# Performance work log

Hardware: AMD Instinct MI355X
Metric: run time of the kernel (lower is better)

Reference implementation:

```python
import jax, jax.numpy as jnp
import numpy as np

N_NODES = 50000
N_EDGES = 800000
HID = 128
LAYERS = 3


def setup_inputs() -> dict:
    key = jax.random.key(0)
    k1, k2, k3, k4 = jax.random.split(key, 4)
    x = jax.random.normal(k1, (N_NODES, HID), dtype=jnp.float32)
    edge_index = jax.random.randint(k2, (2, N_EDGES), 0, N_NODES, dtype=jnp.int64)
    # Glorot-ish scale so 3 stacked layers stay numerically tame
    Ws = jax.random.normal(k3, (LAYERS, HID, HID), dtype=jnp.float32) * (1.0 / np.sqrt(HID))
    bs = jax.random.normal(k4, (LAYERS, HID), dtype=jnp.float32) * 0.01
    return {"x": x, "edge_index": edge_index, "Ws": Ws, "bs": bs}


def reference(x, edge_index, Ws, bs):
    """Stacked GCNConv (add_self_loops=False): out = D^-1/2 A D^-1/2 (x W) + b.
    Returns (final_x, embeddings_list) like the torch module."""
    N = x.shape[0]
    src = edge_index[0]  # message sources (x_j)
    dst = edge_index[1]  # aggregation targets
    # gcn_norm with unit edge weights, no self loops: in-degree on targets
    deg = jax.ops.segment_sum(jnp.ones(src.shape[0], dtype=x.dtype), dst, num_segments=N)
    dinv = jnp.where(deg > 0, jax.lax.rsqrt(jnp.maximum(deg, 1.0)), 0.0).astype(x.dtype)
    norm = dinv[src] * dinv[dst]  # [E]

    embeddings = [x]
    for l in range(Ws.shape[0]):
        h = x @ Ws[l]                               # [N, D] dense transform
        msg = h[src] * norm[:, None]                # [E, D] gather + normalize
        x = jax.ops.segment_sum(msg, dst, num_segments=N) + bs[l]  # scatter-add
        embeddings.append(x)
    return (x, embeddings)
```

## Files before the change

kernel.cpp:

```cpp
#include <hip/hip_runtime.h>

#define N_NODES 50000
#define N_EDGES 800000
#define HID 128
#define SLOT (N_NODES * HID)
#define W_STRIDE (HID * HID)

#define OFF_CNT    0ul
#define OFF_DINV   200192ul
#define OFF_RPTR   400384ul
#define OFF_RFILL  600576ul
#define OFF_BSUM   800768ul
#define OFF_BOFS   801280ul
#define OFF_SRCS   801792ul


__global__ void k_zero_cnt(int* __restrict__ cnt) {
    int i = blockIdx.x * blockDim.x + threadIdx.x;
    if (i < N_NODES) cnt[i] = 0;
}

__global__ void k_count(const int* __restrict__ ei, int* __restrict__ cnt) {
    int e = blockIdx.x * blockDim.x + threadIdx.x;
    if (e < N_EDGES) {
        int d = ei[N_EDGES + e];
        atomicAdd(&cnt[d], 1);
    }
}

__global__ void k_dinv(const int* __restrict__ cnt, float* __restrict__ dinv) {
    int i = blockIdx.x * blockDim.x + threadIdx.x;
    if (i < N_NODES) {
        int c = cnt[i];
        dinv[i] = (c > 0) ? rsqrtf((float)c) : 0.0f;
    }
}

__global__ void k_scan_block(const int* __restrict__ cnt, int* __restrict__ rptr,
                             int* __restrict__ bsum) {
    __shared__ int s[512];
    int tid = threadIdx.x;
    int gid = blockIdx.x * 512 + tid;
    int v = (gid < N_NODES) ? cnt[gid] : 0;
    s[tid] = v;
    __syncthreads();
    for (int off = 1; off < 512; off <<= 1) {
        int t = (tid >= off) ? s[tid - off] : 0;
        __syncthreads();
        s[tid] += t;
        __syncthreads();
    }
    if (gid < N_NODES) rptr[gid] = s[tid] - v;
    if (tid == 511) bsum[blockIdx.x] = s[511];
}

__global__ void k_scan_sums(const int* __restrict__ bsum, int* __restrict__ bofs, int nb) {
    __shared__ int s[128];
    int tid = threadIdx.x;
    int v = (tid < nb) ? bsum[tid] : 0;
    s[tid] = v;
    __syncthreads();
    for (int off = 1; off < 128; off <<= 1) {
        int t = (tid >= off) ? s[tid - off] : 0;
        __syncthreads();
        s[tid] += t;
        __syncthreads();
    }
    if (tid < nb) bofs[tid] = s[tid] - v;
}

__global__ void k_scan_add(int* __restrict__ rptr, int* __restrict__ rfill,
                           const int* __restrict__ bofs) {
    int gid = blockIdx.x * blockDim.x + threadIdx.x;
    if (gid < N_NODES) {
        int r = rptr[gid] + bofs[gid >> 9];
        rptr[gid] = r;
        rfill[gid] = r;
    }
    if (gid == 0) rptr[N_NODES] = N_EDGES;
}

__global__ void k_scatter(const int* __restrict__ ei, int* __restrict__ rfill,
                          int* __restrict__ srcs) {
    int e = blockIdx.x * blockDim.x + threadIdx.x;
    if (e < N_EDGES) {
        int sv = ei[e];
        int d  = ei[N_EDGES + e];
        int pos = atomicAdd(&rfill[d], 1);
        srcs[pos] = sv;
    }
}

__launch_bounds__(256, 2)
__global__ void k_gemm_scale(const float* __restrict__ X, const float* __restrict__ W,
                             const float* __restrict__ dinv, float* __restrict__ H) {
    __shared__ float sX[128 * HID];
    int tid = threadIdx.x;
    int row0 = blockIdx.x * 128;

    const float4* X4  = (const float4*)X;
    float4*       sX4 = (float4*)sX;
    for (int j = tid; j < 4096; j += 256) {
        int r   = j >> 5;
        int c4  = j & 31;
        int row = row0 + r;
        float4 v = {0.f, 0.f, 0.f, 0.f};
        if (row < N_NODES) v = X4[row * 32 + c4];
        sX4[r * 32 + (c4 ^ ((r >> 3) & 7))] = v;
    }
    __syncthreads();

    int ty  = tid >> 4;
    int tx  = tid & 15;
    int swz = ty & 7;

    float4 acc[8][2];
    #pragma unroll
    for (int r = 0; r < 8; ++r) {
        acc[r][0] = {0.f, 0.f, 0.f, 0.f};
        acc[r][1] = {0.f, 0.f, 0.f, 0.f};
    }

    const float4* W4 = (const float4*)W;

    #pragma unroll 2
    for (int k0 = 0; k0 < HID; k0 += 4) {
        int k4 = k0 >> 2;
        float4 xv[8];
        #pragma unroll
        for (int r = 0; r < 8; ++r)
            xv[r] = sX4[(ty * 8 + r) * 32 + (k4 ^ swz)];
        float4 wv[4][2];
        #pragma unroll
        for (int kk = 0; kk < 4; ++kk) {
            wv[kk][0] = W4[(k0 + kk) * 32 + tx * 2 + 0];
            wv[kk][1] = W4[(k0 + kk) * 32 + tx * 2 + 1];
        }
        #pragma unroll
        for (int r = 0; r < 8; ++r) {
            float xk0 = xv[r].x, xk1 = xv[r].y, xk2 = xv[r].z, xk3 = xv[r].w;
            #pragma unroll
            for (int hh = 0; hh < 2; ++hh) {
                acc[r][hh].x += xk0 * wv[0][hh].x + xk1 * wv[1][hh].x + xk2 * wv[2][hh].x + xk3 * wv[3][hh].x;
                acc[r][hh].y += xk0 * wv[0][hh].y + xk1 * wv[1][hh].y + xk2 * wv[2][hh].y + xk3 * wv[3][hh].y;
                acc[r][hh].z += xk0 * wv[0][hh].z + xk1 * wv[1][hh].z + xk2 * wv[2][hh].z + xk3 * wv[3][hh].z;
                acc[r][hh].w += xk0 * wv[0][hh].w + xk1 * wv[1][hh].w + xk2 * wv[2][hh].w + xk3 * wv[3][hh].w;
            }
        }
    }

    float4* H4 = (float4*)H;
    #pragma unroll
    for (int r = 0; r < 8; ++r) {
        int row = row0 + ty * 8 + r;
        if (row < N_NODES) {
            float dv = dinv[row];
            float4 o0 = acc[r][0], o1 = acc[r][1];
            o0.x *= dv; o0.y *= dv; o0.z *= dv; o0.w *= dv;
            o1.x *= dv; o1.y *= dv; o1.z *= dv; o1.w *= dv;
            H4[row * 32 + tx * 2 + 0] = o0;
            H4[row * 32 + tx * 2 + 1] = o1;
        }
    }
}

__global__ void k_agg(const float* __restrict__ H, const int* __restrict__ rptr,
                      const int* __restrict__ srcs, const float* __restrict__ dinv,
                      const float* __restrict__ bias, float* __restrict__ out0) {
    int wid  = (blockIdx.x * blockDim.x + threadIdx.x) >> 6;
    int lane = threadIdx.x & 63;
    if (wid >= N_NODES) return;

    int beg = rptr[wid];
    int end = rptr[wid + 1];

    float2 a0 = {0.f, 0.f}, a1 = {0.f, 0.f}, a2 = {0.f, 0.f}, a3 = {0.f, 0.f};
    int p  = beg;
    int n4 = beg + ((end - beg) & ~3);
    for (; p < n4; p += 4) {
        int s0 = srcs[p + 0];
        int s1 = srcs[p + 1];
        int s2 = srcs[p + 2];
        int s3 = srcs[p + 3];
        float2 h0 = *(const float2*)&H[s0 * HID + lane * 2];
        float2 h1 = *(const float2*)&H[s1 * HID + lane * 2];
        float2 h2 = *(const float2*)&H[s2 * HID + lane * 2];
        float2 h3 = *(const float2*)&H[s3 * HID + lane * 2];
        a0.x += h0.x; a0.y += h0.y;
        a1.x += h1.x; a1.y += h1.y;
        a2.x += h2.x; a2.y += h2.y;
        a3.x += h3.x; a3.y += h3.y;
    }
    for (; p < end; ++p) {
        int s = srcs[p];
        float2 hv = *(const float2*)&H[s * HID + lane * 2];
        a0.x += hv.x; a0.y += hv.y;
    }
    float dv  = dinv[wid];
    float2 bb = *(const float2*)&bias[lane * 2];
    float2 res;
    res.x = (a0.x + a1.x + a2.x + a3.x) * dv + bb.x;
    res.y = (a0.y + a1.y + a2.y + a3.y) * dv + bb.y;
    *(float2*)&out0[wid * HID + lane * 2] = res;
}

__global__ void k_copy(const float* __restrict__ src, float* __restrict__ dst, int n4) {
    int i = blockIdx.x * blockDim.x + threadIdx.x;
    if (i < n4) ((float4*)dst)[i] = ((const float4*)src)[i];
}


extern "C" void kernel_launch(void* const* d_in, const int* in_sizes, int n_in,
                              void* d_out, int out_size, void* d_ws, size_t ws_size,
                              hipStream_t stream) {
    const float* x  = (const float*)d_in[0];
    const int*   ei = (const int*)d_in[1];
    const float* Ws = (const float*)d_in[2];
    const float* bs = (const float*)d_in[3];
    float* out = (float*)d_out;
    char*  ws  = (char*)d_ws;

    int*   cnt   = (int*)  (ws + OFF_CNT);
    float* dinv  = (float*)(ws + OFF_DINV);
    int*   rptr  = (int*)  (ws + OFF_RPTR);
    int*   rfill = (int*)  (ws + OFF_RFILL);
    int*   bsum  = (int*)  (ws + OFF_BSUM);
    int*   bofs  = (int*)  (ws + OFF_BOFS);
    int*   srcs  = (int*)  (ws + OFF_SRCS);

    float* slot0 = out;
    float* slot1 = out + 1l * SLOT;
    float* slot2 = out + 2l * SLOT;
    float* slot3 = out + 3l * SLOT;
    float* slot4 = out + 4l * SLOT;
    float* h     = slot0;

    const int NB_NODE = (N_NODES + 255) / 256;
    const int NB_EDGE = (N_EDGES + 255) / 256;
    const int NB_SCAN = (N_NODES + 511) / 512;

    k_zero_cnt  <<<NB_NODE, 256, 0, stream>>>(cnt);
    k_count     <<<NB_EDGE, 256, 0, stream>>>(ei, cnt);
    k_dinv      <<<NB_NODE, 256, 0, stream>>>(cnt, dinv);
    k_scan_block<<<NB_SCAN, 512, 0, stream>>>(cnt, rptr, bsum);
    k_scan_sums <<<1, 128, 0, stream>>>(bsum, bofs, NB_SCAN);
    k_scan_add  <<<NB_NODE, 256, 0, stream>>>(rptr, rfill, bofs);
    k_scatter   <<<NB_EDGE, 256, 0, stream>>>(ei, rfill, srcs);

    k_copy<<<SLOT / 4 / 256, 256, 0, stream>>>(x, slot1, SLOT / 4);

    const int NB_GEMM = (N_NODES + 127) / 128;
    const int NB_AGG  = (N_NODES + 3) / 4;

    k_gemm_scale<<<NB_GEMM, 256, 0, stream>>>(x, Ws + 0 * W_STRIDE, dinv, h);
    k_agg       <<<NB_AGG, 256, 0, stream>>>(h, rptr, srcs, dinv, bs + 0 * HID, slot2);

    k_gemm_scale<<<NB_GEMM, 256, 0, stream>>>(slot2, Ws + 1 * W_STRIDE, dinv, h);
    k_agg       <<<NB_AGG, 256, 0, stream>>>(h, rptr, srcs, dinv, bs + 1 * HID, slot3);

    k_gemm_scale<<<NB_GEMM, 256, 0, stream>>>(slot3, Ws + 2 * W_STRIDE, dinv, h);
    k_agg       <<<NB_AGG, 256, 0, stream>>>(h, rptr, srcs, dinv, bs + 2 * HID, slot4);
    k_copy<<<SLOT / 4 / 256, 256, 0, stream>>>(slot4, slot0, SLOT / 4);
}
```

Baseline: 428.7 us.

## Use float4 half-wave aggregation, smaller GEMM tiles, and fuse final copy into aggregation

The aggregation kernel now splits each wavefront into two halves that gather float4 rows from different edges, then combines them with a cross-half shuffle. This is meant to raise memory-level parallelism and vector width on the gather. The GEMM tile drops to 64 rows per block with launch bounds of 4 to increase occupancy. When the workspace is large enough, H is placed there, and the last aggregation writes both output slots, which removes the final copy kernel. The cost is extra workspace use and an added fallback branch.

```diff
diff --git a/kernel.cpp b/kernel.cpp
--- a/kernel.cpp
+++ b/kernel.cpp
@@ -13,6 +13,7 @@
 #define OFF_BSUM   800768ul
 #define OFF_BOFS   801280ul
 #define OFF_SRCS   801792ul
+#define OFF_H_WS   4001792ul
 
 
 __global__ void k_zero_cnt(int* __restrict__ cnt) {
@@ -91,16 +92,16 @@
     }
 }
 
-__launch_bounds__(256, 2)
+__launch_bounds__(256, 4)
 __global__ void k_gemm_scale(const float* __restrict__ X, const float* __restrict__ W,
                              const float* __restrict__ dinv, float* __restrict__ H) {
-    __shared__ float sX[128 * HID];
+    __shared__ float sX[64 * HID];
     int tid = threadIdx.x;
-    int row0 = blockIdx.x * 128;
+    int row0 = blockIdx.x * 64;
 
     const float4* X4  = (const float4*)X;
     float4*       sX4 = (float4*)sX;
-    for (int j = tid; j < 4096; j += 256) {
+    for (int j = tid; j < 2048; j += 256) {
         int r   = j >> 5;
         int c4  = j & 31;
         int row = row0 + r;
@@ -112,11 +113,11 @@
 
     int ty  = tid >> 4;
     int tx  = tid & 15;
-    int swz = ty & 7;
-
-    float4 acc[8][2];
+    int swz = (ty >> 1) & 7;
+
+    float4 acc[4][2];
     #pragma unroll
-    for (int r = 0; r < 8; ++r) {
+    for (int r = 0; r < 4; ++r) {
         acc[r][0] = {0.f, 0.f, 0.f, 0.f};
         acc[r][1] = {0.f, 0.f, 0.f, 0.f};
     }
@@ -126,18 +127,18 @@
     #pragma unroll 2
     for (int k0 = 0; k0 < HID; k0 += 4) {
         int k4 = k0 >> 2;
-        float4 xv[8];
-        #pragma unroll
-        for (int r = 0; r < 8; ++r)
-            xv[r] = sX4[(ty * 8 + r) * 32 + (k4 ^ swz)];
         float4 wv[4][2];
         #pragma unroll
         for (int kk = 0; kk < 4; ++kk) {
             wv[kk][0] = W4[(k0 + kk) * 32 + tx * 2 + 0];
             wv[kk][1] = W4[(k0 + kk) * 32 + tx * 2 + 1];
         }
+        float4 xv[4];
         #pragma unroll
-        for (int r = 0; r < 8; ++r) {
+        for (int r = 0; r < 4; ++r)
+            xv[r] = sX4[(ty * 4 + r) * 32 + (k4 ^ swz)];
+        #pragma unroll
+        for (int r = 0; r < 4; ++r) {
             float xk0 = xv[r].x, xk1 = xv[r].y, xk2 = xv[r].z, xk3 = xv[r].w;
             #pragma unroll
             for (int hh = 0; hh < 2; ++hh) {
@@ -151,8 +152,8 @@
 
     float4* H4 = (float4*)H;
     #pragma unroll
-    for (int r = 0; r < 8; ++r) {
-        int row = row0 + ty * 8 + r;
+    for (int r = 0; r < 4; ++r) {
+        int row = row0 + ty * 4 + r;
         if (row < N_NODES) {
             float dv = dinv[row];
             float4 o0 = acc[r][0], o1 = acc[r][1];
@@ -166,42 +167,75 @@
 
 __global__ void k_agg(const float* __restrict__ H, const int* __restrict__ rptr,
                       const int* __restrict__ srcs, const float* __restrict__ dinv,
-                      const float* __restrict__ bias, float* __restrict__ out0) {
+                      const float* __restrict__ bias, float* __restrict__ out0,
+                      float* __restrict__ out1) {
     int wid  = (blockIdx.x * blockDim.x + threadIdx.x) >> 6;
     int lane = threadIdx.x & 63;
     if (wid >= N_NODES) return;
+    int half = lane >> 5;
+    int l32  = lane & 31;
 
     int beg = rptr[wid];
     int end = rptr[wid + 1];
-
-    float2 a0 = {0.f, 0.f}, a1 = {0.f, 0.f}, a2 = {0.f, 0.f}, a3 = {0.f, 0.f};
-    int p  = beg;
-    int n4 = beg + ((end - beg) & ~3);
-    for (; p < n4; p += 4) {
-        int s0 = srcs[p + 0];
-        int s1 = srcs[p + 1];
-        int s2 = srcs[p + 2];
-        int s3 = srcs[p + 3];
-        float2 h0 = *(const float2*)&H[s0 * HID + lane * 2];
-        float2 h1 = *(const float2*)&H[s1 * HID + lane * 2];
-        float2 h2 = *(const float2*)&H[s2 * HID + lane * 2];
-        float2 h3 = *(const float2*)&H[s3 * HID + lane * 2];
-        a0.x += h0.x; a0.y += h0.y;
-        a1.x += h1.x; a1.y += h1.y;
-        a2.x += h2.x; a2.y += h2.y;
-        a3.x += h3.x; a3.y += h3.y;
-    }
-    for (; p < end; ++p) {
-        int s = srcs[p];
-        float2 hv = *(const float2*)&H[s * HID + lane * 2];
-        a0.x += hv.x; a0.y += hv.y;
-    }
-    float dv  = dinv[wid];
-    float2 bb = *(const float2*)&bias[lane * 2];
-    float2 res;
-    res.x = (a0.x + a1.x + a2.x + a3.x) * dv + bb.x;
-    res.y = (a0.y + a1.y + a2.y + a3.y) * dv + bb.y;
-    *(float2*)&out0[wid * HID + lane * 2] = res;
+    int deg = end - beg;
+
+    const float4* H4 = (const float4*)H;
+
+    float4 a0 = {0.f,0.f,0.f,0.f}, a1 = {0.f,0.f,0.f,0.f};
+    float4 a2 = {0.f,0.f,0.f,0.f}, a3 = {0.f,0.f,0.f,0.f};
+
+    int p = beg;
+    int n8 = beg + (deg & ~7);
+    for (; p < n8; p += 8) {
+        int base = p + half * 4;
+        int s0 = srcs[base + 0];
+        int s1 = srcs[base + 1];
+        int s2 = srcs[base + 2];
+        int s3 = srcs[base + 3];
+        float4 h0 = H4[s0 * 32 + l32];
+        float4 h1 = H4[s1 * 32 + l32];
+        float4 h2 = H4[s2 * 32 + l32];
+        float4 h3 = H4[s3 * 32 + l32];
+        a0.x += h0.x; a0.y += h0.y; a0.z += h0.z; a0.w += h0.w;
+        a1.x += h1.x; a1.y += h1.y; a1.z += h1.z; a1.w += h1.w;
+        a2.x += h2.x; a2.y += h2.y; a2.z += h2.z; a2.w += h2.w;
+        a3.x += h3.x; a3.y += h3.y; a3.z += h3.z; a3.w += h3.w;
+    }
+    int rem   = deg & 7;
+    int pairs = rem >> 1;
+    for (int i = 0; i < pairs; ++i) {
+        int e = p + 2 * i + half;
+        float4 hv = H4[srcs[e] * 32 + l32];
+        if (i == 0)      { a0.x += hv.x; a0.y += hv.y; a0.z += hv.z; a0.w += hv.w; }
+        else if (i == 1) { a1.x += hv.x; a1.y += hv.y; a1.z += hv.z; a1.w += hv.w; }
+        else             { a2.x += hv.x; a2.y += hv.y; a2.z += hv.z; a2.w += hv.w; }
+    }
+    if (rem & 1) {
+        float4 hv = H4[srcs[end - 1] * 32 + l32];
+        if (half == 0) { a3.x += hv.x; a3.y += hv.y; a3.z += hv.z; a3.w += hv.w; }
+    }
+
+    float4 s;
+    s.x = a0.x + a1.x + a2.x + a3.x;
+    s.y = a0.y + a1.y + a2.y + a3.y;
+    s.z = a0.z + a1.z + a2.z + a3.z;
+    s.w = a0.w + a1.w + a2.w + a3.w;
+    s.x += __shfl_xor(s.x, 32);
+    s.y += __shfl_xor(s.y, 32);
+    s.z += __shfl_xor(s.z, 32);
+    s.w += __shfl_xor(s.w, 32);
+
+    if (half == 0) {
+        float dv  = dinv[wid];
+        float4 bb = ((const float4*)bias)[l32];
+        float4 res;
+        res.x = s.x * dv + bb.x;
+        res.y = s.y * dv + bb.y;
+        res.z = s.z * dv + bb.z;
+        res.w = s.w * dv + bb.w;
+        ((float4*)out0)[wid * 32 + l32] = res;
+        if (out1) ((float4*)out1)[wid * 32 + l32] = res;
+    }
 }
 
 __global__ void k_copy(const float* __restrict__ src, float* __restrict__ dst, int n4) {
@@ -233,7 +267,9 @@
     float* slot2 = out + 2l * SLOT;
     float* slot3 = out + 3l * SLOT;
     float* slot4 = out + 4l * SLOT;
-    float* h     = slot0;
+
+    bool   h_in_ws = ws_size >= (size_t)(OFF_H_WS + (size_t)SLOT * 4);
+    float* h = h_in_ws ? (float*)(ws + OFF_H_WS) : slot0;
 
     const int NB_NODE = (N_NODES + 255) / 256;
     const int NB_EDGE = (N_EDGES + 255) / 256;
@@ -249,16 +285,20 @@
 
     k_copy<<<SLOT / 4 / 256, 256, 0, stream>>>(x, slot1, SLOT / 4);
 
-    const int NB_GEMM = (N_NODES + 127) / 128;
+    const int NB_GEMM = (N_NODES + 63) / 64;
     const int NB_AGG  = (N_NODES + 3) / 4;
 
     k_gemm_scale<<<NB_GEMM, 256, 0, stream>>>(x, Ws + 0 * W_STRIDE, dinv, h);
-    k_agg       <<<NB_AGG, 256, 0, stream>>>(h, rptr, srcs, dinv, bs + 0 * HID, slot2);
+    k_agg       <<<NB_AGG, 256, 0, stream>>>(h, rptr, srcs, dinv, bs + 0 * HID, slot2, nullptr);
 
     k_gemm_scale<<<NB_GEMM, 256, 0, stream>>>(slot2, Ws + 1 * W_STRIDE, dinv, h);
-    k_agg       <<<NB_AGG, 256, 0, stream>>>(h, rptr, srcs, dinv, bs + 1 * HID, slot3);
+    k_agg       <<<NB_AGG, 256, 0, stream>>>(h, rptr, srcs, dinv, bs + 1 * HID, slot3, nullptr);
 
     k_gemm_scale<<<NB_GEMM, 256, 0, stream>>>(slot3, Ws + 2 * W_STRIDE, dinv, h);
-    k_agg       <<<NB_AGG, 256, 0, stream>>>(h, rptr, srcs, dinv, bs + 2 * HID, slot4);
-    k_copy<<<SLOT / 4 / 256, 256, 0, stream>>>(slot4, slot0, SLOT / 4);
-}
+    if (h_in_ws) {
+        k_agg<<<NB_AGG, 256, 0, stream>>>(h, rptr, srcs, dinv, bs + 2 * HID, slot4, slot0);
+    } else {
+        k_agg<<<NB_AGG, 256, 0, stream>>>(h, rptr, srcs, dinv, bs + 2 * HID, slot4, nullptr);
+        k_copy<<<SLOT / 4 / 256, 256, 0, stream>>>(slot4, slot0, SLOT / 4);
+    }
+}
```

Result: faster. 415.8 us (-3.0%).
